# Performance work log

Measured on AMD Instinct MI355X. Metric: run time of the kernel, lower is better.

The kernel has to match this reference:

```python
import jax, jax.numpy as jnp
import numpy as np

H, W = 2048, 4096
NUM_FRAMES, NUM_CAMERAS = 200, 4


def setup_inputs() -> dict:
    key = jax.random.key(0)
    k0, k1, k2, k3, k4 = jax.random.split(key, 5)
    exposure_params = 0.1 * jax.random.normal(k0, (NUM_FRAMES,), dtype=jnp.float32)
    vignetting_params = 0.05 * jax.random.normal(k1, (NUM_CAMERAS, 3, 5), dtype=jnp.float32)
    color_params = 0.05 * jax.random.normal(k2, (NUM_FRAMES, 8), dtype=jnp.float32)
    crf_params = 0.1 * jax.random.normal(k3, (NUM_CAMERAS, 3, 4), dtype=jnp.float32)
    rgb_in = jax.random.uniform(k4, (H, W, 3), dtype=jnp.float32)
    xs = jnp.arange(W, dtype=jnp.float32) + 0.5  # pixel-center x
    ys = jnp.arange(H, dtype=jnp.float32) + 0.5  # pixel-center y
    gx, gy = jnp.meshgrid(xs, ys)  # each [H, W]
    pixel_coords = jnp.stack([gx, gy], axis=-1)  # [H, W, 2] (x, y)
    return {
        'exposure_params': exposure_params,
        'vignetting_params': vignetting_params,
        'color_params': color_params,
        'crf_params': crf_params,
        'rgb_in': rgb_in,
        'pixel_coords': pixel_coords,
        'resolution_w': W,
        'resolution_h': H,
        'camera_idx': 1,
        'frame_idx': 3,
    }


def _ppisp_forward(exposure_params, vignetting_params, color_params, crf_params,
                   rgb_flat, coords_flat, resolution_w, resolution_h,
                   camera_idx, frame_idx):
    # rgb_flat: [N, 3], coords_flat: [N, 2]
    rgb = rgb_flat
    # --- stage 1: per-frame exposure scale ---
    if frame_idx >= 0:
        rgb = rgb * jnp.exp(exposure_params[frame_idx])
    # --- stage 2: per-camera radial vignetting polynomial (per channel) ---
    if camera_idx >= 0:
        vp = vignetting_params[camera_idx]  # [3, 5] = (cx, cy, a1, a2, a3) per channel
        cx = (0.5 + vp[:, 0]) * resolution_w   # [3] optical center x in pixels
        cy = (0.5 + vp[:, 1]) * resolution_h   # [3]
        norm2 = (0.5 * resolution_w) ** 2 + (0.5 * resolution_h) ** 2
        dx = coords_flat[:, :1] - cx           # [N, 3]
        dy = coords_flat[:, 1:] - cy           # [N, 3]
        r2 = (dx * dx + dy * dy) / norm2       # normalized squared radius
        vig = 1.0 + r2 * (vp[:, 2] + r2 * (vp[:, 3] + r2 * vp[:, 4]))  # Horner cubic in r^2
        rgb = rgb * vig
    # --- stage 3: per-frame 8-param color correction (identity-anchored 3x3) ---
    if frame_idx >= 0:
        p = color_params[frame_idx]  # [8]
        one = jnp.ones((), dtype=p.dtype)
        M = jnp.stack([
            jnp.stack([one + p[0], p[1], p[2]]),
            jnp.stack([p[3], one + p[4], p[5]]),
            jnp.stack([p[6], p[7], one]),
        ])  # [3, 3]
        rgb = rgb @ M.T
    # --- stage 4: per-camera CRF gamma curve (per channel, 4 params) ---
    if camera_idx >= 0:
        q = crf_params[camera_idx]      # [3, 4] = (log_gamma, b1, b2, b3)
        gamma = jnp.exp(q[:, 0])        # [3]
        x = jnp.clip(rgb, 0.0, 1.0)
        y = x ** gamma
        # smooth perturbation anchored at y=0 and y=1
        y = y + y * (1.0 - y) * (q[:, 1] + q[:, 2] * y + q[:, 3] * (1.0 - y))
        rgb = y
    return rgb


def reference(exposure_params, vignetting_params, color_params, crf_params,
              rgb_in, pixel_coords, resolution_w, resolution_h, camera_idx, frame_idx):
    original_shape = rgb_in.shape
    rgb_flat = rgb_in.reshape(-1, 3).astype(jnp.float32)
    coords_flat = pixel_coords.reshape(-1, 2).astype(jnp.float32)
    out = _ppisp_forward(exposure_params.astype(jnp.float32),
                         vignetting_params.astype(jnp.float32),
                         color_params.astype(jnp.float32),
                         crf_params.astype(jnp.float32),
                         rgb_flat, coords_flat,
                         int(resolution_w), int(resolution_h),
                         int(camera_idx), int(frame_idx))
    return out.reshape(original_shape)
```

## Files before the change

kernel.cpp:

```cpp
#include <hip/hip_runtime.h>
#include <math.h>

constexpr int W = 4096;
constexpr int H = 2048;
constexpr int W_SHIFT = 12;
constexpr int NPIX = W * H;
constexpr int NFLOAT = NPIX * 3;
constexpr int FLOATS_PER_THREAD = 12;
constexpr int BLOCK = 256;
constexpr int NTHREADS = NFLOAT / FLOATS_PER_THREAD;
constexpr int GRID = NTHREADS / BLOCK;

struct Params {
    float escale;
    float cx[3], cy[3];
    float a1[3], a2[3], a3[3];
    float inv_norm2;
    float M[9];
    float gamma[3], b1[3], b2[3], b3[3];
    int   crf_on;
};

__global__ __launch_bounds__(BLOCK) void ppisp_kernel(
    const float* __restrict__ exposure,
    const float* __restrict__ vigp,
    const float* __restrict__ colorp,
    const float* __restrict__ crfp,
    const float* __restrict__ rgb_in,
    const int*   __restrict__ cam_idx,
    const int*   __restrict__ frm_idx,
    float*       __restrict__ out)
{
    __shared__ Params s;
    if (threadIdx.x == 0) {
        const int cam = cam_idx[0];
        const int frm = frm_idx[0];
        s.escale = (frm >= 0) ? __expf(exposure[frm]) : 1.0f;
        if (cam >= 0) {
            const float* vp = vigp + cam * 15;
            #pragma unroll
            for (int c = 0; c < 3; ++c) {
                s.cx[c] = (0.5f + vp[c * 5 + 0]) * (float)W;
                s.cy[c] = (0.5f + vp[c * 5 + 1]) * (float)H;
                s.a1[c] = vp[c * 5 + 2];
                s.a2[c] = vp[c * 5 + 3];
                s.a3[c] = vp[c * 5 + 4];
            }
        } else {
            #pragma unroll
            for (int c = 0; c < 3; ++c) {
                s.cx[c] = s.cy[c] = 0.0f;
                s.a1[c] = s.a2[c] = s.a3[c] = 0.0f;
            }
        }
        const float nx = 0.5f * (float)W, ny = 0.5f * (float)H;
        s.inv_norm2 = 1.0f / (nx * nx + ny * ny);
        if (frm >= 0) {
            const float* p = colorp + frm * 8;
            s.M[0] = 1.0f + p[0]; s.M[1] = p[1];        s.M[2] = p[2];
            s.M[3] = p[3];        s.M[4] = 1.0f + p[4]; s.M[5] = p[5];
            s.M[6] = p[6];        s.M[7] = p[7];        s.M[8] = 1.0f;
        } else {
            s.M[0] = 1.0f; s.M[1] = 0.0f; s.M[2] = 0.0f;
            s.M[3] = 0.0f; s.M[4] = 1.0f; s.M[5] = 0.0f;
            s.M[6] = 0.0f; s.M[7] = 0.0f; s.M[8] = 1.0f;
        }
        if (cam >= 0) {
            s.crf_on = 1;
            const float* q = crfp + cam * 12;
            #pragma unroll
            for (int c = 0; c < 3; ++c) {
                s.gamma[c] = __expf(q[c * 4 + 0]);
                s.b1[c] = q[c * 4 + 1];
                s.b2[c] = q[c * 4 + 2];
                s.b3[c] = q[c * 4 + 3];
            }
        } else {
            s.crf_on = 0;
        }
    }
    __syncthreads();

    const float escale = s.escale;
    const float inv_norm2 = s.inv_norm2;
    float cx[3], cy[3], a1[3], a2[3], a3[3], gam[3], b1[3], b2[3], b3[3];
    #pragma unroll
    for (int c = 0; c < 3; ++c) {
        cx[c] = s.cx[c]; cy[c] = s.cy[c];
        a1[c] = s.a1[c]; a2[c] = s.a2[c]; a3[c] = s.a3[c];
        gam[c] = s.gamma[c]; b1[c] = s.b1[c]; b2[c] = s.b2[c]; b3[c] = s.b3[c];
    }
    float M[9];
    #pragma unroll
    for (int i = 0; i < 9; ++i) M[i] = s.M[i];
    const int crf_on = s.crf_on;

    const int tid = blockIdx.x * BLOCK + threadIdx.x;

    const float4* __restrict__ in4 = (const float4*)rgb_in;
    float4* __restrict__ out4 = (float4*)out;
    float4 f0 = in4[tid * 3 + 0];
    float4 f1 = in4[tid * 3 + 1];
    float4 f2 = in4[tid * 3 + 2];

    float v[12] = {f0.x, f0.y, f0.z, f0.w,
                   f1.x, f1.y, f1.z, f1.w,
                   f2.x, f2.y, f2.z, f2.w};

    const int p0 = tid * 4;
    #pragma unroll
    for (int k = 0; k < 4; ++k) {
        const int p = p0 + k;
        const float px = (float)(p & (W - 1)) + 0.5f;
        const float py = (float)(p >> W_SHIFT) + 0.5f;

        float ch[3];
        #pragma unroll
        for (int c = 0; c < 3; ++c) ch[c] = v[k * 3 + c] * escale;

        #pragma unroll
        for (int c = 0; c < 3; ++c) {
            const float dx = px - cx[c];
            const float dy = py - cy[c];
            const float r2 = (dx * dx + dy * dy) * inv_norm2;
            const float vg = 1.0f + r2 * (a1[c] + r2 * (a2[c] + r2 * a3[c]));
            ch[c] *= vg;
        }

        float o[3];
        o[0] = M[0] * ch[0] + M[1] * ch[1] + M[2] * ch[2];
        o[1] = M[3] * ch[0] + M[4] * ch[1] + M[5] * ch[2];
        o[2] = M[6] * ch[0] + M[7] * ch[1] + M[8] * ch[2];

        if (crf_on) {
            #pragma unroll
            for (int c = 0; c < 3; ++c) {
                const float x = fminf(fmaxf(o[c], 0.0f), 1.0f);
                float y = exp2f(gam[c] * __log2f(x));
                y = y + y * (1.0f - y) * (b1[c] + b2[c] * y + b3[c] * (1.0f - y));
                o[c] = y;
            }
        }

        v[k * 3 + 0] = o[0];
        v[k * 3 + 1] = o[1];
        v[k * 3 + 2] = o[2];
    }

    out4[tid * 3 + 0] = make_float4(v[0], v[1], v[2], v[3]);
    out4[tid * 3 + 1] = make_float4(v[4], v[5], v[6], v[7]);
    out4[tid * 3 + 2] = make_float4(v[8], v[9], v[10], v[11]);
}

extern "C" void kernel_launch(void* const* d_in, const int* in_sizes, int n_in,
                              void* d_out, int out_size, void* d_ws, size_t ws_size,
                              hipStream_t stream) {
    const float* exposure = (const float*)d_in[0];
    const float* vigp     = (const float*)d_in[1];
    const float* colorp   = (const float*)d_in[2];
    const float* crfp     = (const float*)d_in[3];
    const float* rgb_in   = (const float*)d_in[4];
    const int* cam_idx = (const int*)d_in[8];
    const int* frm_idx = (const int*)d_in[9];
    float* out = (float*)d_out;

    ppisp_kernel<<<dim3(GRID), dim3(BLOCK), 0, stream>>>(
        exposure, vigp, colorp, crfp, rgb_in, cam_idx, frm_idx, out);
}
```

Before: 230.5 us.

## Stage pixels through LDS with async global_load_lds and compute params per thread

Each block now loads its whole tile into LDS using asynchronous global_load_lds with fully coalesced per-wave 16-byte accesses. Threads then process 8 pixels each out of LDS and write results back to LDS, and a coalesced store copies the tile to global memory. The thread-0 parameter setup and its shared struct are gone: every thread loads the parameters itself, overlapping with the async copy. The aim is better coalescing and overlap of parameter setup with input loads, at the cost of 24KB of LDS per block (lower occupancy), a second barrier, and strided LDS reads that may hit bank conflicts.

Result: faster. 223.8 us (-2.9%).

```diff
diff --git a/kernel.cpp b/kernel.cpp
--- a/kernel.cpp
+++ b/kernel.cpp
@@ -6,20 +6,15 @@
 constexpr int W_SHIFT = 12;
 constexpr int NPIX = W * H;
 constexpr int NFLOAT = NPIX * 3;
-constexpr int FLOATS_PER_THREAD = 12;
 constexpr int BLOCK = 256;
-constexpr int NTHREADS = NFLOAT / FLOATS_PER_THREAD;
-constexpr int GRID = NTHREADS / BLOCK;
+constexpr int PIX_PER_THREAD = 8;
+constexpr int FLT_PER_THREAD = 3 * PIX_PER_THREAD;
+constexpr int FLT_PER_BLOCK = BLOCK * FLT_PER_THREAD;
+constexpr int FLT_PER_WAVE = 64 * FLT_PER_THREAD;
+constexpr int GRID = NFLOAT / FLT_PER_BLOCK;
 
-struct Params {
-    float escale;
-    float cx[3], cy[3];
-    float a1[3], a2[3], a3[3];
-    float inv_norm2;
-    float M[9];
-    float gamma[3], b1[3], b2[3], b3[3];
-    int   crf_on;
-};
+#define AS1 __attribute__((address_space(1)))
+#define AS3 __attribute__((address_space(3)))
 
 __global__ __launch_bounds__(BLOCK) void ppisp_kernel(
     const float* __restrict__ exposure,
@@ -31,85 +26,92 @@
     const int*   __restrict__ frm_idx,
     float*       __restrict__ out)
 {
-    __shared__ Params s;
-    if (threadIdx.x == 0) {
-        const int cam = cam_idx[0];
-        const int frm = frm_idx[0];
-        s.escale = (frm >= 0) ? __expf(exposure[frm]) : 1.0f;
-        if (cam >= 0) {
-            const float* vp = vigp + cam * 15;
-            #pragma unroll
-            for (int c = 0; c < 3; ++c) {
-                s.cx[c] = (0.5f + vp[c * 5 + 0]) * (float)W;
-                s.cy[c] = (0.5f + vp[c * 5 + 1]) * (float)H;
-                s.a1[c] = vp[c * 5 + 2];
-                s.a2[c] = vp[c * 5 + 3];
-                s.a3[c] = vp[c * 5 + 4];
-            }
-        } else {
-            #pragma unroll
-            for (int c = 0; c < 3; ++c) {
-                s.cx[c] = s.cy[c] = 0.0f;
-                s.a1[c] = s.a2[c] = s.a3[c] = 0.0f;
-            }
-        }
-        const float nx = 0.5f * (float)W, ny = 0.5f * (float)H;
-        s.inv_norm2 = 1.0f / (nx * nx + ny * ny);
-        if (frm >= 0) {
-            const float* p = colorp + frm * 8;
-            s.M[0] = 1.0f + p[0]; s.M[1] = p[1];        s.M[2] = p[2];
-            s.M[3] = p[3];        s.M[4] = 1.0f + p[4]; s.M[5] = p[5];
-            s.M[6] = p[6];        s.M[7] = p[7];        s.M[8] = 1.0f;
-        } else {
-            s.M[0] = 1.0f; s.M[1] = 0.0f; s.M[2] = 0.0f;
-            s.M[3] = 0.0f; s.M[4] = 1.0f; s.M[5] = 0.0f;
-            s.M[6] = 0.0f; s.M[7] = 0.0f; s.M[8] = 1.0f;
-        }
-        if (cam >= 0) {
-            s.crf_on = 1;
-            const float* q = crfp + cam * 12;
-            #pragma unroll
-            for (int c = 0; c < 3; ++c) {
-                s.gamma[c] = __expf(q[c * 4 + 0]);
-                s.b1[c] = q[c * 4 + 1];
-                s.b2[c] = q[c * 4 + 2];
-                s.b3[c] = q[c * 4 + 3];
-            }
-        } else {
-            s.crf_on = 0;
+    __shared__ float smem[FLT_PER_BLOCK];
+
+    const int t    = threadIdx.x;
+    const int wave = t >> 6;
+    const int lane = t & 63;
+
+    {
+        const float* gw = rgb_in + (size_t)blockIdx.x * FLT_PER_BLOCK
+                                 + wave * FLT_PER_WAVE;
+        #pragma unroll
+        for (int j = 0; j < 6; ++j) {
+            const float* g = gw + j * 256 + lane * 4;
+            const float* l = &smem[wave * FLT_PER_WAVE + j * 256 + lane * 4];
+            __builtin_amdgcn_global_load_lds((const AS1 void*)g, (AS3 void*)l,
+                                             16, 0, 0);
         }
     }
+
+    const int cam = __builtin_amdgcn_readfirstlane(cam_idx[0]);
+    const int frm = __builtin_amdgcn_readfirstlane(frm_idx[0]);
+
+    const float escale = (frm >= 0) ? __expf(exposure[frm]) : 1.0f;
+
+    float cx[3], cy[3], a1[3], a2[3], a3[3];
+    if (cam >= 0) {
+        const float* vp = vigp + cam * 15;
+        #pragma unroll
+        for (int c = 0; c < 3; ++c) {
+            cx[c] = (0.5f + vp[c * 5 + 0]) * (float)W;
+            cy[c] = (0.5f + vp[c * 5 + 1]) * (float)H;
+            a1[c] = vp[c * 5 + 2];
+            a2[c] = vp[c * 5 + 3];
+            a3[c] = vp[c * 5 + 4];
+        }
+    } else {
+        #pragma unroll
+        for (int c = 0; c < 3; ++c) {
+            cx[c] = cy[c] = 0.0f;
+            a1[c] = a2[c] = a3[c] = 0.0f;
+        }
+    }
+    const float nx = 0.5f * (float)W, ny = 0.5f * (float)H;
+    const float inv_norm2 = 1.0f / (nx * nx + ny * ny);
+
+    float M[9];
+    if (frm >= 0) {
+        const float* p = colorp + frm * 8;
+        M[0] = 1.0f + p[0]; M[1] = p[1];        M[2] = p[2];
+        M[3] = p[3];        M[4] = 1.0f + p[4]; M[5] = p[5];
+        M[6] = p[6];        M[7] = p[7];        M[8] = 1.0f;
+    } else {
+        M[0] = 1.0f; M[1] = 0.0f; M[2] = 0.0f;
+        M[3] = 0.0f; M[4] = 1.0f; M[5] = 0.0f;
+        M[6] = 0.0f; M[7] = 0.0f; M[8] = 1.0f;
+    }
+
+    float gam[3], b1[3], b2[3], b3[3];
+    const int crf_on = (cam >= 0);
+    if (crf_on) {
+        const float* q = crfp + cam * 12;
+        #pragma unroll
+        for (int c = 0; c < 3; ++c) {
+            gam[c] = __expf(q[c * 4 + 0]);
+            b1[c]  = q[c * 4 + 1];
+            b2[c]  = q[c * 4 + 2];
+            b3[c]  = q[c * 4 + 3];
+        }
+    } else {
+        #pragma unroll
+        for (int c = 0; c < 3; ++c) { gam[c] = 1.0f; b1[c] = b2[c] = b3[c] = 0.0f; }
+    }
+
     __syncthreads();
 
-    const float escale = s.escale;
-    const float inv_norm2 = s.inv_norm2;
-    float cx[3], cy[3], a1[3], a2[3], a3[3], gam[3], b1[3], b2[3], b3[3];
+    float4* s4 = (float4*)smem;
+    float v[FLT_PER_THREAD];
     #pragma unroll
-    for (int c = 0; c < 3; ++c) {
-        cx[c] = s.cx[c]; cy[c] = s.cy[c];
-        a1[c] = s.a1[c]; a2[c] = s.a2[c]; a3[c] = s.a3[c];
-        gam[c] = s.gamma[c]; b1[c] = s.b1[c]; b2[c] = s.b2[c]; b3[c] = s.b3[c];
+    for (int j = 0; j < 6; ++j) {
+        const float4 x = s4[t * 6 + j];
+        v[4 * j + 0] = x.x; v[4 * j + 1] = x.y;
+        v[4 * j + 2] = x.z; v[4 * j + 3] = x.w;
     }
-    float M[9];
+
+    const int p0 = blockIdx.x * (FLT_PER_BLOCK / 3) + t * PIX_PER_THREAD;
     #pragma unroll
-    for (int i = 0; i < 9; ++i) M[i] = s.M[i];
-    const int crf_on = s.crf_on;
-
-    const int tid = blockIdx.x * BLOCK + threadIdx.x;
-
-    const float4* __restrict__ in4 = (const float4*)rgb_in;
-    float4* __restrict__ out4 = (float4*)out;
-    float4 f0 = in4[tid * 3 + 0];
-    float4 f1 = in4[tid * 3 + 1];
-    float4 f2 = in4[tid * 3 + 2];
-
-    float v[12] = {f0.x, f0.y, f0.z, f0.w,
-                   f1.x, f1.y, f1.z, f1.w,
-                   f2.x, f2.y, f2.z, f2.w};
-
-    const int p0 = tid * 4;
-    #pragma unroll
-    for (int k = 0; k < 4; ++k) {
+    for (int k = 0; k < PIX_PER_THREAD; ++k) {
         const int p = p0 + k;
         const float px = (float)(p & (W - 1)) + 0.5f;
         const float py = (float)(p >> W_SHIFT) + 0.5f;
@@ -123,8 +125,7 @@
             const float dx = px - cx[c];
             const float dy = py - cy[c];
             const float r2 = (dx * dx + dy * dy) * inv_norm2;
-            const float vg = 1.0f + r2 * (a1[c] + r2 * (a2[c] + r2 * a3[c]));
-            ch[c] *= vg;
+            ch[c] *= 1.0f + r2 * (a1[c] + r2 * (a2[c] + r2 * a3[c]));
         }
 
         float o[3];
@@ -147,9 +148,22 @@
         v[k * 3 + 2] = o[2];
     }
 
-    out4[tid * 3 + 0] = make_float4(v[0], v[1], v[2], v[3]);
-    out4[tid * 3 + 1] = make_float4(v[4], v[5], v[6], v[7]);
-    out4[tid * 3 + 2] = make_float4(v[8], v[9], v[10], v[11]);
+    #pragma unroll
+    for (int j = 0; j < 6; ++j)
+        s4[t * 6 + j] = make_float4(v[4 * j + 0], v[4 * j + 1],
+                                    v[4 * j + 2], v[4 * j + 3]);
+
+    __syncthreads();
+
+    {
+        float4* out4 = (float4*)out + (size_t)blockIdx.x * (FLT_PER_BLOCK / 4);
+        const int base = wave * (FLT_PER_WAVE / 4);
+        #pragma unroll
+        for (int j = 0; j < 6; ++j) {
+            const int idx = base + j * 64 + lane;
+            out4[idx] = s4[idx];
+        }
+    }
 }
 
 extern "C" void kernel_launch(void* const* d_in, const int* in_sizes, int n_in,
```
